# Performance work log

Measured on AMD Instinct MI355X. Metric: run time of the kernel, lower is better.

The kernel has to match this reference:

```python
import jax, jax.numpy as jnp
import numpy as np

N, D, DFF, E, F, K, H = 4096, 512, 512, 512, 4096, 1024, 4


def _rn(i, shape, s=0.02):
    return jax.random.normal(jax.random.fold_in(jax.random.key(0), i), shape, dtype=jnp.float32) * s


def setup_inputs():
    inp = {"inputs": jax.random.normal(jax.random.key(1), (N, D), dtype=jnp.float32)}
    i = 10
    for p in ("enc", "dec"):
        for nm, shp in (("wq", (D, D)), ("wk", (D, D)), ("wv", (D, D)), ("wo", (D, D)), ("w1", (D, DFF)), ("w2", (DFF, D))):
            inp[p + "_" + nm] = _rn(i, shp); i += 1
        for nm, shp in (("bq", (D,)), ("bk", (D,)), ("bv", (D,)), ("bo", (D,)), ("b1", (DFF,)), ("b2", (D,))):
            inp[p + "_" + nm] = jnp.zeros(shp, jnp.float32)
        inp[p + "_ln1_g"] = jnp.ones((D,), jnp.float32)
        inp[p + "_ln1_b"] = jnp.zeros((D,), jnp.float32)
        inp[p + "_ln2_g"] = jnp.ones((D,), jnp.float32)
        inp[p + "_ln2_b"] = jnp.zeros((D,), jnp.float32)
    inp["fc1_w"] = _rn(100, (D, E))
    inp["fc1_b"] = jnp.zeros((E,), jnp.float32)
    inp["fc2_w"] = _rn(101, (D, F))
    inp["fc2_b"] = jnp.zeros((F,), jnp.float32)
    inp["emb"] = _rn(102, (K, E), s=0.01)
    return inp


def layer_norm(x, g, b, eps=1e-6):
    mu = jnp.mean(x, axis=-1, keepdims=True)
    var = jnp.mean(jnp.square(x - mu), axis=-1, keepdims=True)
    return (x - mu) * jax.lax.rsqrt(var + eps) * g + b


def row_distance(a, b):
    # cosine similarity between rows (sim in [-1,1]; loss maps (sim+1)/2 -> [0,1])
    an = a * jax.lax.rsqrt(jnp.maximum(jnp.sum(a * a, axis=1, keepdims=True), 1e-12))
    bn = b * jax.lax.rsqrt(jnp.maximum(jnp.sum(b * b, axis=1, keepdims=True), 1e-12))
    return an @ bn.T


def nearest_context(feature, context):
    distances = row_distance(feature, context) * -1.0  # [N, K]
    min_ind = jnp.argmin(distances, axis=1)
    one_hot = jax.nn.one_hot(min_ind, context.shape[0], dtype=jnp.float32)  # [N, K]
    rslt = one_hot @ jax.lax.stop_gradient(context)  # [N, E]
    return rslt, one_hot


@jax.custom_vjp
def vq(feature, context):
    return nearest_context(feature, context)[0]


def _vq_fwd(feature, context):
    value, ind = nearest_context(feature, context)
    return value, ind


def _vq_bwd(ind, d_value):
    # straight-through to feature, scatter-add (via one-hot matmul) to codebook
    return d_value, ind.T @ d_value


vq.defvjp(_vq_fwd, _vq_bwd)


def encoder_layer(x, wq, bq, wk, bk, wv, bv, wo, bo, w1, b1, w2, b2, g1, be1, g2, be2):
    n, d = x.shape
    dh = d // H
    q = (x @ wq + bq).reshape(n, H, dh)
    k = (x @ wk + bk).reshape(n, H, dh)
    v = (x @ wv + bv).reshape(n, H, dh)
    scores = jnp.einsum('nhd,mhd->hnm', q, k) / jnp.sqrt(jnp.float32(dh))
    attn = jax.nn.softmax(scores, axis=-1)
    ctx = jnp.einsum('hnm,mhd->nhd', attn, v).reshape(n, d)
    out1 = layer_norm(x + (ctx @ wo + bo), g1, be1)
    ffn = jax.nn.relu(out1 @ w1 + b1) @ w2 + b2
    return layer_norm(out1 + ffn, g2, be2)


def reference(inputs, enc_wq, enc_wk, enc_wv, enc_wo, enc_w1, enc_w2, enc_bq, enc_bk, enc_bv, enc_bo, enc_b1, enc_b2, enc_ln1_g, enc_ln1_b, enc_ln2_g, enc_ln2_b, dec_wq, dec_wk, dec_wv, dec_wo, dec_w1, dec_w2, dec_bq, dec_bk, dec_bv, dec_bo, dec_b1, dec_b2, dec_ln1_g, dec_ln1_b, dec_ln2_g, dec_ln2_b, fc1_w, fc1_b, fc2_w, fc2_b, emb):
    encoded = encoder_layer(inputs, enc_wq, enc_bq, enc_wk, enc_bk, enc_wv, enc_bv, enc_wo, enc_bo, enc_w1, enc_b1, enc_w2, enc_b2, enc_ln1_g, enc_ln1_b, enc_ln2_g, enc_ln2_b)
    encoded = encoded @ fc1_w + fc1_b  # [N, E]
    vq_feat = vq(encoded, emb)
    _, context_ind = nearest_context(encoded, emb)
    decoded = encoder_layer(vq_feat, dec_wq, dec_bq, dec_wk, dec_bk, dec_wv, dec_bv, dec_wo, dec_bo, dec_w1, dec_b1, dec_w2, dec_b2, dec_ln1_g, dec_ln1_b, dec_ln2_g, dec_ln2_b)
    decoded = jax.nn.relu(decoded @ fc2_w + fc2_b)  # [N, F]
    return encoded, vq_feat, context_ind, decoded, emb
```

## Files before the change

### kernel.cpp

```cpp
#include <hip/hip_runtime.h>
#include <hip/hip_bf16.h>
#include <stdint.h>

typedef __bf16 bf16;
typedef __bf16 bf16x8 __attribute__((ext_vector_type(8)));
typedef float  f32x4v __attribute__((ext_vector_type(4)));

__device__ __forceinline__ void cvt8(const float* v, bf16x8& hh, bf16x8& ll) {
    #pragma unroll
    for (int j = 0; j < 8; j++) {
        bf16 b = (bf16)v[j]; hh[j] = b; ll[j] = (bf16)(v[j] - (float)b);
    }
}

__device__ __forceinline__ float block_reduce_sum256(float v) {
    __shared__ float red[256];
    int tid = threadIdx.x;
    red[tid] = v; __syncthreads();
    #pragma unroll
    for (int s = 128; s > 0; s >>= 1) {
        if (tid < s) red[tid] += red[tid + s];
        __syncthreads();
    }
    float r = red[0]; __syncthreads();
    return r;
}

template<int BMT, bool RELU, bool TRANS, bool BNAT, bool HILO>
__global__ __launch_bounds__(256, 2)
void gemm3(const float* __restrict__ A, const float* __restrict__ B,
           const float* __restrict__ bias, float* __restrict__ C,
           bf16* __restrict__ Chi, bf16* __restrict__ Clo,
           int K, int lda, int ldb, int ldc, float alpha)
{
    constexpr int BN = 128, TK = 32;
    constexpr int RM = BMT / 32;
    __shared__ __align__(16) bf16 Ah[BMT * TK];
    __shared__ __align__(16) bf16 Al[BMT * TK];
    __shared__ __align__(16) bf16 Bh[BN * TK];
    __shared__ __align__(16) bf16 Bl[BN * TK];

    const int tid  = threadIdx.x;
    const int wave = tid >> 6, lane = tid & 63;
    const int wr = wave >> 1, wc = wave & 1;
    const long bm = (long)blockIdx.y * BMT;
    const long bn = (long)blockIdx.x * BN;
    const int fr = lane & 15, fq = lane >> 4;

    f32x4v acc[RM][4] = {};

    for (int k0 = 0; k0 < K; k0 += TK) {
        #pragma unroll
        for (int it = 0; it < BMT / 64; it++) {
            const int c = it * 256 + tid;
            const int r = c >> 2, k8 = c & 3;
            const float* src = A + (bm + r) * (long)lda + k0 + k8 * 8;
            float4 f0 = ((const float4*)src)[0], f1 = ((const float4*)src)[1];
            float v[8] = {f0.x, f0.y, f0.z, f0.w, f1.x, f1.y, f1.z, f1.w};
            bf16x8 hh, ll; cvt8(v, hh, ll);
            *(bf16x8*)&Ah[r * TK + k8 * 8] = hh;
            *(bf16x8*)&Al[r * TK + k8 * 8] = ll;
        }
        if (BNAT) {
            const int col = tid & 127, bkh = (tid >> 7) * 16;
            const float* src = B + (long)(k0 + bkh) * ldb + bn + col;
            float v[16];
            #pragma unroll
            for (int kk = 0; kk < 16; kk++) v[kk] = src[(long)kk * ldb];
            bf16x8 h0, l0, h1, l1; cvt8(v, h0, l0); cvt8(v + 8, h1, l1);
            bf16* hd = &Bh[col * TK + bkh];
            bf16* ld_ = &Bl[col * TK + bkh];
            ((bf16x8*)hd)[0] = h0; ((bf16x8*)hd)[1] = h1;
            ((bf16x8*)ld_)[0] = l0; ((bf16x8*)ld_)[1] = l1;
        } else {
            #pragma unroll
            for (int it = 0; it < 2; it++) {
                const int c = it * 256 + tid;
                const int r = c >> 2, k8 = c & 3;
                const float* src = B + (bn + r) * (long)ldb + k0 + k8 * 8;
                float4 f0 = ((const float4*)src)[0], f1 = ((const float4*)src)[1];
                float v[8] = {f0.x, f0.y, f0.z, f0.w, f1.x, f1.y, f1.z, f1.w};
                bf16x8 hh, ll; cvt8(v, hh, ll);
                *(bf16x8*)&Bh[r * TK + k8 * 8] = hh;
                *(bf16x8*)&Bl[r * TK + k8 * 8] = ll;
            }
        }
        __syncthreads();

        bf16x8 ah[RM], am[RM], bh[4], bm_[4];
        #pragma unroll
        for (int i = 0; i < RM; i++) {
            const int r = (wr * (BMT / 2) + i * 16 + fr) * TK + fq * 8;
            ah[i] = *(const bf16x8*)&Ah[r];
            am[i] = *(const bf16x8*)&Al[r];
        }
        #pragma unroll
        for (int j = 0; j < 4; j++) {
            const int r = (wc * 64 + j * 16 + fr) * TK + fq * 8;
            bh[j] = *(const bf16x8*)&Bh[r];
            bm_[j] = *(const bf16x8*)&Bl[r];
        }
        #pragma unroll
        for (int i = 0; i < RM; i++)
            #pragma unroll
            for (int j = 0; j < 4; j++) {
                acc[i][j] = __builtin_amdgcn_mfma_f32_16x16x32_bf16(am[i], bh[j], acc[i][j], 0, 0, 0);
                acc[i][j] = __builtin_amdgcn_mfma_f32_16x16x32_bf16(ah[i], bm_[j], acc[i][j], 0, 0, 0);
                acc[i][j] = __builtin_amdgcn_mfma_f32_16x16x32_bf16(ah[i], bh[j], acc[i][j], 0, 0, 0);
            }
        __syncthreads();
    }

    #pragma unroll
    for (int i = 0; i < RM; i++) {
        #pragma unroll
        for (int j = 0; j < 4; j++) {
            const long col = bn + wc * 64 + j * 16 + fr;
            const float bv = bias ? bias[col] : 0.f;
            #pragma unroll
            for (int r = 0; r < 4; r++) {
                const long row = bm + wr * (BMT / 2) + i * 16 + fq * 4 + r;
                float v = acc[i][j][r] * alpha + bv;
                if (RELU) v = fmaxf(v, 0.f);
                const long idx = TRANS ? (col * (long)ldc + row) : (row * (long)ldc + col);
                if (HILO) {
                    bf16 hh = (bf16)v;
                    Chi[idx] = hh;
                    Clo[idx] = (bf16)(v - (float)hh);
                } else {
                    C[idx] = v;
                }
            }
        }
    }
}

__global__ __launch_bounds__(256, 2)
void qkv_gemm(const float* __restrict__ X,
              const float* __restrict__ Wq, const float* __restrict__ Wk, const float* __restrict__ Wv,
              const float* __restrict__ Bq, const float* __restrict__ Bk, const float* __restrict__ Bv,
              float* __restrict__ Qo, bf16* __restrict__ Khi, bf16* __restrict__ Klo,
              bf16* __restrict__ Vthi, bf16* __restrict__ Vtlo)
{
    constexpr int TK = 32, D = 512, N = 4096;
    __shared__ __align__(16) bf16 Ah[64 * TK];
    __shared__ __align__(16) bf16 Al[64 * TK];
    __shared__ __align__(16) bf16 Bh[128 * TK];
    __shared__ __align__(16) bf16 Bl[128 * TK];

    const int tid  = threadIdx.x;
    const int wave = tid >> 6, lane = tid & 63;
    const int wr = wave >> 1, wc = wave & 1;
    const int sel = blockIdx.x >> 2, wcol0 = (blockIdx.x & 3) * 128;
    const long bm = (long)blockIdx.y * 64;
    const int fr = lane & 15, fq = lane >> 4;

    const float* W  = sel == 0 ? Wq : (sel == 1 ? Wk : Wv);
    const float* Bb = sel == 0 ? Bq : (sel == 1 ? Bk : Bv);

    f32x4v acc[2][4] = {};

    for (int k0 = 0; k0 < D; k0 += TK) {
        {
            const int r = tid >> 2, k8 = tid & 3;
            const float* src = X + (bm + r) * (long)D + k0 + k8 * 8;
            float4 f0 = ((const float4*)src)[0], f1 = ((const float4*)src)[1];
            float v[8] = {f0.x, f0.y, f0.z, f0.w, f1.x, f1.y, f1.z, f1.w};
            bf16x8 hh, ll; cvt8(v, hh, ll);
            *(bf16x8*)&Ah[r * TK + k8 * 8] = hh;
            *(bf16x8*)&Al[r * TK + k8 * 8] = ll;
        }
        {
            const int col = tid & 127, bkh = (tid >> 7) * 16;
            const float* src = W + (long)(k0 + bkh) * D + wcol0 + col;
            float v[16];
            #pragma unroll
            for (int kk = 0; kk < 16; kk++) v[kk] = src[(long)kk * D];
            bf16x8 h0, l0, h1, l1; cvt8(v, h0, l0); cvt8(v + 8, h1, l1);
            bf16* hd = &Bh[col * TK + bkh];
            bf16* ld_ = &Bl[col * TK + bkh];
            ((bf16x8*)hd)[0] = h0; ((bf16x8*)hd)[1] = h1;
            ((bf16x8*)ld_)[0] = l0; ((bf16x8*)ld_)[1] = l1;
        }
        __syncthreads();

        bf16x8 ah[2], am[2], bh[4], bm_[4];
        #pragma unroll
        for (int i = 0; i < 2; i++) {
            const int r = (wr * 32 + i * 16 + fr) * TK + fq * 8;
            ah[i] = *(const bf16x8*)&Ah[r];
            am[i] = *(const bf16x8*)&Al[r];
        }
        #pragma unroll
        for (int j = 0; j < 4; j++) {
            const int r = (wc * 64 + j * 16 + fr) * TK + fq * 8;
            bh[j] = *(const bf16x8*)&Bh[r];
            bm_[j] = *(const bf16x8*)&Bl[r];
        }
        #pragma unroll
        for (int i = 0; i < 2; i++)
            #pragma unroll
            for (int j = 0; j < 4; j++) {
                acc[i][j] = __builtin_amdgcn_mfma_f32_16x16x32_bf16(am[i], bh[j], acc[i][j], 0, 0, 0);
                acc[i][j] = __builtin_amdgcn_mfma_f32_16x16x32_bf16(ah[i], bm_[j], acc[i][j], 0, 0, 0);
                acc[i][j] = __builtin_amdgcn_mfma_f32_16x16x32_bf16(ah[i], bh[j], acc[i][j], 0, 0, 0);
            }
        __syncthreads();
    }

    #pragma unroll
    for (int i = 0; i < 2; i++) {
        #pragma unroll
        for (int j = 0; j < 4; j++) {
            const int col = wc * 64 + j * 16 + fr;
            const float bv = Bb[wcol0 + col];
            #pragma unroll
            for (int r = 0; r < 4; r++) {
                const long row = bm + wr * 32 + i * 16 + fq * 4 + r;
                const float v = acc[i][j][r] + bv;
                if (sel == 0) {
                    Qo[row * D + wcol0 + col] = v;
                } else {
                    const bf16 hh = (bf16)v;
                    const bf16 ll = (bf16)(v - (float)hh);
                    const long idx = (sel == 1) ? (row * (long)D + wcol0 + col)
                                                : ((long)(wcol0 + col) * N + row);
                    if (sel == 1) { Khi[idx] = hh; Klo[idx] = ll; }
                    else          { Vthi[idx] = hh; Vtlo[idx] = ll; }
                }
            }
        }
    }
}

__global__ __launch_bounds__(256, 2)
void flash_attn(const float* __restrict__ Q,
                const bf16* __restrict__ Khi, const bf16* __restrict__ Klo,
                const bf16* __restrict__ Vthi, const bf16* __restrict__ Vtlo,
                float* __restrict__ Op, float* __restrict__ ml)
{
    constexpr int N = 4096, D = 512, SPAN = 1024;
    constexpr float TS = 0.12751791f;
    constexpr int PSTR = 68;

    __shared__ __align__(16) bf16 smem[32768];
    bf16* Kh = smem;
    bf16* Kl = smem + 8192;
    bf16* Vh = smem + 16384;
    bf16* Vl = smem + 24576;

    const int tid = threadIdx.x;
    const int wave = tid >> 6, lane = tid & 63;
    const int fr = lane & 15, fq = lane >> 4;
    const int qt = blockIdx.x, h = blockIdx.y, s = blockIdx.z;
    const long q0 = (long)qt * 128;

    float* Pf = (float*)smem + wave * (16 * PSTR);

    bf16x8 qh[2][4], ql[2][4];
    #pragma unroll
    for (int rg = 0; rg < 2; rg++)
        #pragma unroll
        for (int kt = 0; kt < 4; kt++) {
            const float* src = Q + (q0 + wave * 32 + rg * 16 + fr) * D + h * 128 + kt * 32 + fq * 8;
            float4 f0 = ((const float4*)src)[0], f1 = ((const float4*)src)[1];
            float v[8] = {f0.x, f0.y, f0.z, f0.w, f1.x, f1.y, f1.z, f1.w};
            cvt8(v, qh[rg][kt], ql[rg][kt]);
        }

    f32x4v o[2][8] = {};
    float m_run[2][4], l_run[2][4];
    #pragma unroll
    for (int rg = 0; rg < 2; rg++)
        #pragma unroll
        for (int r = 0; r < 4; r++) { m_run[rg][r] = -1e30f; l_run[rg][r] = 0.f; }

    for (int j0 = s * SPAN; j0 < (s + 1) * SPAN; j0 += 64) {
        __syncthreads();
        #pragma unroll
        for (int g = 0; g < 4; g++) {
            const int cid = g * 256 + tid;
            const int n = cid >> 4, k8 = cid & 15;
            const long gsrc = (long)(j0 + n) * D + h * 128 + k8 * 8;
            const int off = n * 128 + ((k8 ^ (n & 15)) << 3);
            *(bf16x8*)&Kh[off] = *(const bf16x8*)&Khi[gsrc];
            *(bf16x8*)&Kl[off] = *(const bf16x8*)&Klo[gsrc];
        }
        #pragma unroll
        for (int g = 0; g < 4; g++) {
            const int cid = g * 256 + tid;
            const int d = cid >> 3, k8 = cid & 7;
            const long gsrc = (long)(h * 128 + d) * N + j0 + k8 * 8;
            const int off = d * 64 + ((k8 ^ (d & 7)) << 3);
            *(bf16x8*)&Vh[off] = *(const bf16x8*)&Vthi[gsrc];
            *(bf16x8*)&Vl[off] = *(const bf16x8*)&Vtlo[gsrc];
        }
        __syncthreads();

        f32x4v sacc[2][4] = {};
        #pragma unroll
        for (int jb = 0; jb < 4; jb++) {
            bf16x8 kh[4], km[4];
            #pragma unroll
            for (int kt = 0; kt < 4; kt++) {
                const int col = jb * 16 + fr;
                const int k8 = kt * 4 + fq;
                const int off = col * 128 + ((k8 ^ (col & 15)) << 3);
                kh[kt] = *(const bf16x8*)&Kh[off];
                km[kt] = *(const bf16x8*)&Kl[off];
            }
            #pragma unroll
            for (int kt = 0; kt < 4; kt++)
                #pragma unroll
                for (int rg = 0; rg < 2; rg++) {
                    sacc[rg][jb] = __builtin_amdgcn_mfma_f32_16x16x32_bf16(ql[rg][kt], kh[kt], sacc[rg][jb], 0, 0, 0);
                    sacc[rg][jb] = __builtin_amdgcn_mfma_f32_16x16x32_bf16(qh[rg][kt], km[kt], sacc[rg][jb], 0, 0, 0);
                    sacc[rg][jb] = __builtin_amdgcn_mfma_f32_16x16x32_bf16(qh[rg][kt], kh[kt], sacc[rg][jb], 0, 0, 0);
                }
        }

        float t[2][4][4], alpha_[2][4], rs[2][4];
        #pragma unroll
        for (int rg = 0; rg < 2; rg++) {
            float mloc[4];
            #pragma unroll
            for (int r = 0; r < 4; r++) {
                float a = sacc[rg][0][r] * TS, b = sacc[rg][1][r] * TS;
                float c = sacc[rg][2][r] * TS, d2 = sacc[rg][3][r] * TS;
                t[rg][0][r] = a; t[rg][1][r] = b; t[rg][2][r] = c; t[rg][3][r] = d2;
                mloc[r] = fmaxf(fmaxf(a, b), fmaxf(c, d2));
            }
            #pragma unroll
            for (int bmask = 1; bmask <= 8; bmask <<= 1)
                #pragma unroll
                for (int r = 0; r < 4; r++)
                    mloc[r] = fmaxf(mloc[r], __shfl_xor(mloc[r], bmask));
            #pragma unroll
            for (int r = 0; r < 4; r++) {
                const float mn = fmaxf(m_run[rg][r], mloc[r]);
                alpha_[rg][r] = exp2f(m_run[rg][r] - mn);
                m_run[rg][r] = mn;
                rs[rg][r] = 0.f;
            }
        }
        __syncthreads();

        bf16x8 ph[2][2], pl[2][2];
        #pragma unroll
        for (int rg = 0; rg < 2; rg++) {
            #pragma unroll
            for (int jb = 0; jb < 4; jb++)
                #pragma unroll
                for (int r = 0; r < 4; r++) {
                    const float p = exp2f(t[rg][jb][r] - m_run[rg][r]);
                    rs[rg][r] += p;
                    Pf[(fq * 4 + r) * PSTR + jb * 16 + fr] = p;
                }
            #pragma unroll
            for (int bmask = 1; bmask <= 8; bmask <<= 1)
                #pragma unroll
                for (int r = 0; r < 4; r++)
                    rs[rg][r] += __shfl_xor(rs[rg][r], bmask);
            #pragma unroll
            for (int r = 0; r < 4; r++)
                l_run[rg][r] = l_run[rg][r] * alpha_[rg][r] + rs[rg][r];
            #pragma unroll
            for (int kt = 0; kt < 2; kt++) {
                const float* base = &Pf[fr * PSTR + kt * 32 + fq * 8];
                float4 f0 = ((const float4*)base)[0], f1 = ((const float4*)base)[1];
                float v[8] = {f0.x, f0.y, f0.z, f0.w, f1.x, f1.y, f1.z, f1.w};
                cvt8(v, ph[rg][kt], pl[rg][kt]);
            }
        }
        #pragma unroll
        for (int rg = 0; rg < 2; rg++)
            #pragma unroll
            for (int jbo = 0; jbo < 8; jbo++)
                #pragma unroll
                for (int r = 0; r < 4; r++)
                    o[rg][jbo][r] *= alpha_[rg][r];

        #pragma unroll
        for (int jbo = 0; jbo < 8; jbo++) {
            bf16x8 vh_[2], vl_[2];
            #pragma unroll
            for (int kt = 0; kt < 2; kt++) {
                const int col = jbo * 16 + fr;
                const int k8 = kt * 4 + fq;
                const int off = col * 64 + ((k8 ^ (col & 7)) << 3);
                vh_[kt] = *(const bf16x8*)&Vh[off];
                vl_[kt] = *(const bf16x8*)&Vl[off];
            }
            #pragma unroll
            for (int rg = 0; rg < 2; rg++)
                #pragma unroll
                for (int kt = 0; kt < 2; kt++) {
                    o[rg][jbo] = __builtin_amdgcn_mfma_f32_16x16x32_bf16(pl[rg][kt], vh_[kt], o[rg][jbo], 0, 0, 0);
                    o[rg][jbo] = __builtin_amdgcn_mfma_f32_16x16x32_bf16(ph[rg][kt], vl_[kt], o[rg][jbo], 0, 0, 0);
                    o[rg][jbo] = __builtin_amdgcn_mfma_f32_16x16x32_bf16(ph[rg][kt], vh_[kt], o[rg][jbo], 0, 0, 0);
                }
        }
    }

    const long sidx = (long)((h * 32 + qt) * 4 + s);
    float* ob = Op + sidx * 16384;
    #pragma unroll
    for (int rg = 0; rg < 2; rg++)
        #pragma unroll
        for (int jbo = 0; jbo < 8; jbo++)
            #pragma unroll
            for (int r = 0; r < 4; r++) {
                const int lrow = wave * 32 + rg * 16 + fq * 4 + r;
                ob[lrow * 128 + jbo * 16 + fr] = o[rg][jbo][r];
            }
    if (fr == 0) {
        #pragma unroll
        for (int rg = 0; rg < 2; rg++)
            #pragma unroll
            for (int r = 0; r < 4; r++) {
                const int lrow = wave * 32 + rg * 16 + fq * 4 + r;
                ml[sidx * 256 + lrow]       = m_run[rg][r];
                ml[sidx * 256 + 128 + lrow] = l_run[rg][r];
            }
    }
}

__global__ void flash_merge(const float* __restrict__ Op, const float* __restrict__ ml,
                            float* __restrict__ ctx)
{
    const int idx = blockIdx.x;
    const int h = idx >> 5, qt = idx & 31;
    const int tid = threadIdx.x;
    __shared__ float es[4][128], il[128];
    if (tid < 128) {
        float m[4], l[4];
        #pragma unroll
        for (int s = 0; s < 4; s++) {
            m[s] = ml[(long)(idx * 4 + s) * 256 + tid];
            l[s] = ml[(long)(idx * 4 + s) * 256 + 128 + tid];
        }
        float mx = fmaxf(fmaxf(m[0], m[1]), fmaxf(m[2], m[3]));
        float denom = 0.f;
        #pragma unroll
        for (int s = 0; s < 4; s++) {
            const float e = exp2f(m[s] - mx);
            es[s][tid] = e;
            denom += e * l[s];
        }
        il[tid] = 1.f / denom;
    }
    __syncthreads();
    const long b = (long)idx * 4 * 16384;
    #pragma unroll
    for (int i = 0; i < 64; i++) {
        const int e = tid + i * 256;
        const int row = e >> 7, col = e & 127;
        float v = es[0][row] * Op[b + e] + es[1][row] * Op[b + 16384 + e]
                + es[2][row] * Op[b + 32768 + e] + es[3][row] * Op[b + 49152 + e];
        ctx[(long)(qt * 128 + row) * 512 + h * 128 + col] = v * il[row];
    }
}

__global__ void add_ln_f32(const float* __restrict__ a, const float* __restrict__ b,
                           const float* __restrict__ g, const float* __restrict__ be,
                           float* __restrict__ out)
{
    const long row = blockIdx.x;
    const int tid = threadIdx.x;
    const long base = row * 512L;
    float x0 = a[base + tid]       + b[base + tid];
    float x1 = a[base + tid + 256] + b[base + tid + 256];
    float s = block_reduce_sum256(x0 + x1);
    float mu = s * (1.f / 512.f);
    float d0 = x0 - mu, d1 = x1 - mu;
    float var = block_reduce_sum256(d0 * d0 + d1 * d1) * (1.f / 512.f);
    float invs = rsqrtf(var + 1e-6f);
    out[base + tid]       = d0 * invs * g[tid]       + be[tid];
    out[base + tid + 256] = d1 * invs * g[tid + 256] + be[tid + 256];
}

__global__ void normalize_emb(const float* __restrict__ emb, float* __restrict__ embn)
{
    const long row = blockIdx.x;
    const int tid = threadIdx.x;
    const long base = row * 512L;
    float a0 = emb[base + tid];
    float a1 = emb[base + tid + 256];
    float ss = block_reduce_sum256(a0 * a0 + a1 * a1);
    float sc = rsqrtf(fmaxf(ss, 1e-12f));
    embn[base + tid]       = a0 * sc;
    embn[base + tid + 256] = a1 * sc;
}

__global__ void vq_select_onehot(float* __restrict__ sims, const float* __restrict__ emb,
                                 float* __restrict__ vq_out)
{
    __shared__ float sv[256];
    __shared__ int   si[256];
    const long row = blockIdx.x;
    const int tid = threadIdx.x;
    float* s = sims + row * 1024L;
    float v0 = s[tid], v1 = s[tid + 256], v2 = s[tid + 512], v3 = s[tid + 768];
    float best = v0; int bi = tid;
    if (v1 > best) { best = v1; bi = tid + 256; }
    if (v2 > best) { best = v2; bi = tid + 512; }
    if (v3 > best) { best = v3; bi = tid + 768; }
    sv[tid] = best; si[tid] = bi; __syncthreads();
    #pragma unroll
    for (int st = 128; st > 0; st >>= 1) {
        if (tid < st) {
            if (sv[tid + st] > sv[tid] ||
                (sv[tid + st] == sv[tid] && si[tid + st] < si[tid])) {
                sv[tid] = sv[tid + st]; si[tid] = si[tid + st];
            }
        }
        __syncthreads();
    }
    const int idx = si[0];
    s[tid]       = (tid       == idx) ? 1.f : 0.f;
    s[tid + 256] = (tid + 256 == idx) ? 1.f : 0.f;
    s[tid + 512] = (tid + 512 == idx) ? 1.f : 0.f;
    s[tid + 768] = (tid + 768 == idx) ? 1.f : 0.f;
    const float* er = emb + (long)idx * 512;
    float* vr = vq_out + row * 512L;
    vr[tid]       = er[tid];
    vr[tid + 256] = er[tid + 256];
}

struct EncW {
    const float *wq, *wk, *wv, *wo, *w1, *w2;
    const float *bq, *bk, *bv, *bo, *b1, *b2;
    const float *g1, *be1, *g2, *be2;
};

static void run_encoder_g3(hipStream_t stream, const float* x, const EncW& w,
                           float* qb, bf16* khi, bf16* klo, bf16* vthi, bf16* vtlo,
                           float* ctx, float* Op, float* ml,
                           float* x1, float* hb, float* out)
{
    const int N = 4096, D = 512;
    qkv_gemm<<<dim3(12, 64), 256, 0, stream>>>(
        x, w.wq, w.wk, w.wv, w.bq, w.bk, w.bv, qb, khi, klo, vthi, vtlo);
    flash_attn<<<dim3(32, 4, 4), 256, 0, stream>>>(qb, khi, klo, vthi, vtlo, Op, ml);
    flash_merge<<<128, 256, 0, stream>>>(Op, ml, ctx);
    gemm3<64, false, false, true, false><<<dim3(4, 64), 256, 0, stream>>>(
        ctx, w.wo, w.bo, qb, nullptr, nullptr, D, D, D, D, 1.f);
    add_ln_f32<<<N, 256, 0, stream>>>(x, qb, w.g1, w.be1, x1);
    gemm3<64, true, false, true, false><<<dim3(4, 64), 256, 0, stream>>>(
        x1, w.w1, w.b1, hb, nullptr, nullptr, D, D, D, D, 1.f);
    gemm3<64, false, false, true, false><<<dim3(4, 64), 256, 0, stream>>>(
        hb, w.w2, w.b2, qb, nullptr, nullptr, D, D, D, D, 1.f);
    add_ln_f32<<<N, 256, 0, stream>>>(x1, qb, w.g2, w.be2, out);
}

extern "C" void kernel_launch(void* const* d_in, const int* in_sizes, int n_in,
                              void* d_out, int out_size, void* d_ws, size_t ws_size,
                              hipStream_t stream)
{
    const int N = 4096, D = 512, E = 512, F = 4096, KCB = 1024;
    (void)in_sizes; (void)n_in; (void)out_size; (void)d_ws; (void)ws_size;

    const float* x_in  = (const float*)d_in[0];
    const float* fc1_w = (const float*)d_in[33];
    const float* fc1_b = (const float*)d_in[34];
    const float* fc2_w = (const float*)d_in[35];
    const float* fc2_b = (const float*)d_in[36];
    const float* emb   = (const float*)d_in[37];

    float* out0 = (float*)d_out;
    float* out1 = out0 + (size_t)N * E;
    float* out2 = out1 + (size_t)N * E;
    float* out3 = out2 + (size_t)N * KCB;
    float* out4 = out3 + (size_t)N * F;

    char* arena = (char*)out3;
    const size_t MB = 1024 * 1024;
    float* qb     = (float*)(arena + 0 * MB);
    bf16*  khi    = (bf16*) (arena + 8 * MB);
    bf16*  klo    = (bf16*) (arena + 12 * MB);
    bf16*  vthi   = (bf16*) (arena + 16 * MB);
    bf16*  vtlo   = (bf16*) (arena + 20 * MB);
    float* ctx    = (float*)(arena + 24 * MB);
    float* Op     = (float*)(arena + 32 * MB);
    float* decout = (float*)(arena + 56 * MB);
    float* x1     = (float*)(arena + 16 * MB);
    float* hb     = (float*)(arena + 8 * MB);
    float* ml     = (float*)out4;
    float* embn   = out1;
    float* stage  = (float*)out4;

    EncW ew = { (const float*)d_in[1],  (const float*)d_in[2],  (const float*)d_in[3],
                (const float*)d_in[4],  (const float*)d_in[5],  (const float*)d_in[6],
                (const float*)d_in[7],  (const float*)d_in[8],  (const float*)d_in[9],
                (const float*)d_in[10], (const float*)d_in[11], (const float*)d_in[12],
                (const float*)d_in[13], (const float*)d_in[14], (const float*)d_in[15],
                (const float*)d_in[16] };
    EncW dw = { (const float*)d_in[17], (const float*)d_in[18], (const float*)d_in[19],
                (const float*)d_in[20], (const float*)d_in[21], (const float*)d_in[22],
                (const float*)d_in[23], (const float*)d_in[24], (const float*)d_in[25],
                (const float*)d_in[26], (const float*)d_in[27], (const float*)d_in[28],
                (const float*)d_in[29], (const float*)d_in[30], (const float*)d_in[31],
                (const float*)d_in[32] };

    normalize_emb<<<KCB, 256, 0, stream>>>(emb, embn);
    run_encoder_g3(stream, x_in, ew, qb, khi, klo, vthi, vtlo, ctx, Op, ml, x1, hb, ctx);

    gemm3<64, false, false, true, false><<<dim3(4, 64), 256, 0, stream>>>(
        ctx, fc1_w, fc1_b, out0, nullptr, nullptr, D, D, E, E, 1.f);

    gemm3<128, false, false, false, false><<<dim3(8, 32), 256, 0, stream>>>(
        out0, embn, nullptr, out2, nullptr, nullptr, E, E, E, KCB, 1.f);
    vq_select_onehot<<<N, 256, 0, stream>>>(out2, emb, out1);

    run_encoder_g3(stream, out1, dw, qb, khi, klo, vthi, vtlo, ctx, Op, ml, x1, hb, decout);

    hipMemcpyAsync(stage, decout + (size_t)3584 * D, (size_t)512 * D * sizeof(float),
                   hipMemcpyDeviceToDevice, stream);
    gemm3<128, true, false, true, false><<<dim3(F / 128, 3584 / 128), 256, 0, stream>>>(
        decout, fc2_w, fc2_b, out3, nullptr, nullptr, D, D, F, F, 1.f);
    gemm3<128, true, false, true, false><<<dim3(F / 128, 512 / 128), 256, 0, stream>>>(
        stage, fc2_w, fc2_b, out3 + (size_t)3584 * F, nullptr, nullptr, D, D, F, F, 1.f);

    hipMemcpyAsync(out4, emb, (size_t)KCB * E * sizeof(float), hipMemcpyDeviceToDevice, stream);
}
```

Measured before the change: 964.7 us.

## Double-buffer K/V tiles with register prefetch in flash attention, shrink KV tile

```diff
diff --git a/kernel.cpp b/kernel.cpp
--- a/kernel.cpp
+++ b/kernel.cpp
@@ -239,15 +239,11 @@
                 const bf16* __restrict__ Vthi, const bf16* __restrict__ Vtlo,
                 float* __restrict__ Op, float* __restrict__ ml)
 {
-    constexpr int N = 4096, D = 512, SPAN = 1024;
+    constexpr int N = 4096, D = 512, SPAN = 1024, TKV = 32, NT = SPAN / TKV;
     constexpr float TS = 0.12751791f;
-    constexpr int PSTR = 68;
-
-    __shared__ __align__(16) bf16 smem[32768];
-    bf16* Kh = smem;
-    bf16* Kl = smem + 8192;
-    bf16* Vh = smem + 16384;
-    bf16* Vl = smem + 24576;
+    constexpr int PSTR = 36;
+
+    __shared__ __align__(16) bf16 smem[37376];
 
     const int tid = threadIdx.x;
     const int wave = tid >> 6, lane = tid & 63;
@@ -255,7 +251,16 @@
     const int qt = blockIdx.x, h = blockIdx.y, s = blockIdx.z;
     const long q0 = (long)qt * 128;
 
-    float* Pf = (float*)smem + wave * (16 * PSTR);
+    float* Pf = (float*)(smem + 32768) + wave * (16 * PSTR);
+
+    const int kn0 = tid >> 4, kk8 = tid & 15;
+    const int vd0 = tid >> 2, vk8 = tid & 3;
+    const int ko_[2] = { kn0 * 128 + ((kk8 ^ (kn0 & 15)) << 3),
+                         (kn0 + 16) * 128 + ((kk8 ^ ((kn0 + 16) & 15)) << 3) };
+    const int vo_[2] = { vd0 * 32 + ((vk8 ^ ((vd0 >> 2) & 3)) << 3),
+                         (vd0 + 64) * 32 + ((vk8 ^ (((vd0 + 64) >> 2) & 3)) << 3) };
+
+    uint4 rkh[2], rkl[2], rvh[2], rvl[2];
 
     bf16x8 qh[2][4], ql[2][4];
     #pragma unroll
@@ -275,40 +280,64 @@
         #pragma unroll
         for (int r = 0; r < 4; r++) { m_run[rg][r] = -1e30f; l_run[rg][r] = 0.f; }
 
-    for (int j0 = s * SPAN; j0 < (s + 1) * SPAN; j0 += 64) {
+    const int j0base = s * SPAN;
+
+    {
+        const int j0 = j0base;
+        #pragma unroll
+        for (int it = 0; it < 2; it++) {
+            const long kg = (long)(j0 + kn0 + it * 16) * D + h * 128 + kk8 * 8;
+            rkh[it] = *(const uint4*)&Khi[kg];
+            rkl[it] = *(const uint4*)&Klo[kg];
+            const long vg = (long)(h * 128 + vd0 + it * 64) * N + j0 + vk8 * 8;
+            rvh[it] = *(const uint4*)&Vthi[vg];
+            rvl[it] = *(const uint4*)&Vtlo[vg];
+        }
+    }
+
+    #pragma unroll 2
+    for (int jt = 0; jt < NT; jt++) {
+        bf16* buf = smem + ((jt & 1) << 14);
+        bf16* Kh = buf;
+        bf16* Kl = buf + 4096;
+        bf16* Vh = buf + 8192;
+        bf16* Vl = buf + 12288;
+
+        #pragma unroll
+        for (int it = 0; it < 2; it++) {
+            *(uint4*)&Kh[ko_[it]] = rkh[it];
+            *(uint4*)&Kl[ko_[it]] = rkl[it];
+            *(uint4*)&Vh[vo_[it]] = rvh[it];
+            *(uint4*)&Vl[vo_[it]] = rvl[it];
+        }
         __syncthreads();
-        #pragma unroll
-        for (int g = 0; g < 4; g++) {
-            const int cid = g * 256 + tid;
-            const int n = cid >> 4, k8 = cid & 15;
-            const long gsrc = (long)(j0 + n) * D + h * 128 + k8 * 8;
-            const int off = n * 128 + ((k8 ^ (n & 15)) << 3);
-            *(bf16x8*)&Kh[off] = *(const bf16x8*)&Khi[gsrc];
-            *(bf16x8*)&Kl[off] = *(const bf16x8*)&Klo[gsrc];
-        }
-        #pragma unroll
-        for (int g = 0; g < 4; g++) {
-            const int cid = g * 256 + tid;
-            const int d = cid >> 3, k8 = cid & 7;
-            const long gsrc = (long)(h * 128 + d) * N + j0 + k8 * 8;
-            const int off = d * 64 + ((k8 ^ (d & 7)) << 3);
-            *(bf16x8*)&Vh[off] = *(const bf16x8*)&Vthi[gsrc];
-            *(bf16x8*)&Vl[off] = *(const bf16x8*)&Vtlo[gsrc];
-        }
-        __syncthreads();
-
-        f32x4v sacc[2][4] = {};
-        #pragma unroll
-        for (int jb = 0; jb < 4; jb++) {
+
+        if (jt + 1 < NT) {
+            const int j0 = j0base + (jt + 1) * TKV;
+            #pragma unroll
+            for (int it = 0; it < 2; it++) {
+                const long kg = (long)(j0 + kn0 + it * 16) * D + h * 128 + kk8 * 8;
+                rkh[it] = *(const uint4*)&Khi[kg];
+                rkl[it] = *(const uint4*)&Klo[kg];
+                const long vg = (long)(h * 128 + vd0 + it * 64) * N + j0 + vk8 * 8;
+                rvh[it] = *(const uint4*)&Vthi[vg];
+                rvl[it] = *(const uint4*)&Vtlo[vg];
+            }
+        }
+
+        f32x4v sacc[2][2] = {};
+        #pragma unroll
+        for (int jb = 0; jb < 2; jb++) {
             bf16x8 kh[4], km[4];
             #pragma unroll
             for (int kt = 0; kt < 4; kt++) {
                 const int col = jb * 16 + fr;
                 const int k8 = kt * 4 + fq;
-                const int off = col * 128 + ((k8 ^ (col & 15)) << 3);
+                const int off = col * 128 + ((k8 ^ fr) << 3);
                 kh[kt] = *(const bf16x8*)&Kh[off];
                 km[kt] = *(const bf16x8*)&Kl[off];
             }
+            __builtin_amdgcn_s_setprio(1);
             #pragma unroll
             for (int kt = 0; kt < 4; kt++)
                 #pragma unroll
@@ -317,18 +346,18 @@
                     sacc[rg][jb] = __builtin_amdgcn_mfma_f32_16x16x32_bf16(qh[rg][kt], km[kt], sacc[rg][jb], 0, 0, 0);
                     sacc[rg][jb] = __builtin_amdgcn_mfma_f32_16x16x32_bf16(qh[rg][kt], kh[kt], sacc[rg][jb], 0, 0, 0);
                 }
-        }
-
-        float t[2][4][4], alpha_[2][4], rs[2][4];
+            __builtin_amdgcn_s_setprio(0);
+        }
+
+        float t[2][2][4], alpha_[2][4], rs[2][4];
         #pragma unroll
         for (int rg = 0; rg < 2; rg++) {
             float mloc[4];
             #pragma unroll
             for (int r = 0; r < 4; r++) {
                 float a = sacc[rg][0][r] * TS, b = sacc[rg][1][r] * TS;
-                float c = sacc[rg][2][r] * TS, d2 = sacc[rg][3][r] * TS;
-                t[rg][0][r] = a; t[rg][1][r] = b; t[rg][2][r] = c; t[rg][3][r] = d2;
-                mloc[r] = fmaxf(fmaxf(a, b), fmaxf(c, d2));
+                t[rg][0][r] = a; t[rg][1][r] = b;
+                mloc[r] = fmaxf(a, b);
             }
             #pragma unroll
             for (int bmask = 1; bmask <= 8; bmask <<= 1)
@@ -343,13 +372,12 @@
                 rs[rg][r] = 0.f;
             }
         }
-        __syncthreads();
-
-        bf16x8 ph[2][2], pl[2][2];
+
+        bf16x8 ph[2], pl[2];
         #pragma unroll
         for (int rg = 0; rg < 2; rg++) {
             #pragma unroll
-            for (int jb = 0; jb < 4; jb++)
+            for (int jb = 0; jb < 2; jb++)
                 #pragma unroll
                 for (int r = 0; r < 4; r++) {
                     const float p = exp2f(t[rg][jb][r] - m_run[rg][r]);
@@ -364,14 +392,14 @@
             #pragma unroll
             for (int r = 0; r < 4; r++)
                 l_run[rg][r] = l_run[rg][r] * alpha_[rg][r] + rs[rg][r];
-            #pragma unroll
-            for (int kt = 0; kt < 2; kt++) {
-                const float* base = &Pf[fr * PSTR + kt * 32 + fq * 8];
+            {
+                const float* base = &Pf[fr * PSTR + fq * 8];
                 float4 f0 = ((const float4*)base)[0], f1 = ((const float4*)base)[1];
                 float v[8] = {f0.x, f0.y, f0.z, f0.w, f1.x, f1.y, f1.z, f1.w};
-                cvt8(v, ph[rg][kt], pl[rg][kt]);
-            }
-        }
+                cvt8(v, ph[rg], pl[rg]);
+            }
+        }
+
         #pragma unroll
         for (int rg = 0; rg < 2; rg++)
             #pragma unroll
@@ -382,23 +410,18 @@
 
         #pragma unroll
         for (int jbo = 0; jbo < 8; jbo++) {
-            bf16x8 vh_[2], vl_[2];
-            #pragma unroll
-            for (int kt = 0; kt < 2; kt++) {
-                const int col = jbo * 16 + fr;
-                const int k8 = kt * 4 + fq;
-                const int off = col * 64 + ((k8 ^ (col & 7)) << 3);
-                vh_[kt] = *(const bf16x8*)&Vh[off];
-                vl_[kt] = *(const bf16x8*)&Vl[off];
-            }
-            #pragma unroll
-            for (int rg = 0; rg < 2; rg++)
-                #pragma unroll
-                for (int kt = 0; kt < 2; kt++) {
-                    o[rg][jbo] = __builtin_amdgcn_mfma_f32_16x16x32_bf16(pl[rg][kt], vh_[kt], o[rg][jbo], 0, 0, 0);
-                    o[rg][jbo] = __builtin_amdgcn_mfma_f32_16x16x32_bf16(ph[rg][kt], vl_[kt], o[rg][jbo], 0, 0, 0);
-                    o[rg][jbo] = __builtin_amdgcn_mfma_f32_16x16x32_bf16(ph[rg][kt], vh_[kt], o[rg][jbo], 0, 0, 0);
-                }
+            const int col = jbo * 16 + fr;
+            const int off = col * 32 + ((fq ^ ((fr >> 2) & 3)) << 3);
+            bf16x8 vh_ = *(const bf16x8*)&Vh[off];
+            bf16x8 vl_ = *(const bf16x8*)&Vl[off];
+            __builtin_amdgcn_s_setprio(1);
+            #pragma unroll
+            for (int rg = 0; rg < 2; rg++) {
+                o[rg][jbo] = __builtin_amdgcn_mfma_f32_16x16x32_bf16(pl[rg], vh_, o[rg][jbo], 0, 0, 0);
+                o[rg][jbo] = __builtin_amdgcn_mfma_f32_16x16x32_bf16(ph[rg], vl_, o[rg][jbo], 0, 0, 0);
+                o[rg][jbo] = __builtin_amdgcn_mfma_f32_16x16x32_bf16(ph[rg], vh_, o[rg][jbo], 0, 0, 0);
+            }
+            __builtin_amdgcn_s_setprio(0);
         }
     }
 
```

Measured after the change: 1.020 ms. +5.7%, slower.
